# Performance work log

Measured on AMD Instinct MI355X. Metric: run time of the kernel, lower is better.

The kernel has to match this reference:

```python
import jax, jax.numpy as jnp
import numpy as np
import math

D, H = 128, 8
B, LC, LQ = 8, 512, 64


def pos_signal(channels, length):
    # tensor2tensor timing signal, returned as [C, L]
    pos = jnp.arange(length, dtype=jnp.float32)
    nts = channels // 2
    inc = math.log(1.0e4) / (nts - 1)
    inv = jnp.exp(jnp.arange(nts, dtype=jnp.float32) * -inc)
    st = pos[:, None] * inv[None, :]                      # [L, nts]
    sig = jnp.concatenate([jnp.sin(st), jnp.cos(st)], 1)  # [L, C]
    return sig.T


def mask_logits(t, m):
    return t * m + (1.0 - m) * -1e30


def ln_c(x, g, b):  # LayerNorm over channel dim of [B, D, L]
    mu = jnp.mean(x, axis=1, keepdims=True)
    var = jnp.mean((x - mu) ** 2, axis=1, keepdims=True)
    return (x - mu) / jnp.sqrt(var + 1e-5) * g[None, :, None] + b[None, :, None]


def conv1x1(x, w, b=None):  # x [B, I, L], w [O, I]
    y = jnp.einsum('oi,bil->bol', w, x)
    return y if b is None else y + b[None, :, None]


def dw_sep_conv(x, dw, pw, pwb):  # depthwise (k, no bias) -> pointwise (bias) -> relu
    k = dw.shape[-1]
    y = jax.lax.conv_general_dilated(x, dw[:, None, :], (1,), [(k // 2, k // 2)],
        dimension_numbers=('NCH', 'OIH', 'NCH'), feature_group_count=x.shape[1])
    return jax.nn.relu(conv1x1(y, pw, pwb))


def self_attention(x, mem_w, q_w, mask, n_head):  # x [B, D, L]
    b, d, L = x.shape
    dh = d // n_head
    mem = jnp.einsum('oi,bil->blo', mem_w, x)  # [B, L, 2D]
    q = jnp.einsum('oi,bil->blo', q_w, x)      # [B, L, D]
    def heads(t):
        return t.reshape(b, L, n_head, dh).transpose(0, 2, 1, 3)  # [B, H, L, dh]
    Qh = heads(q) * dh ** -0.5
    K = heads(mem[..., :d])
    V = heads(mem[..., d:])
    logits = jnp.einsum('bhqe,bhke->bhqk', Qh, K)
    logits = mask_logits(logits, mask[:, None, None, :])
    w = jax.nn.softmax(logits, axis=-1)
    o = jnp.einsum('bhqk,bhke->bhqe', w, V)
    return o.transpose(0, 2, 1, 3).reshape(b, L, d).transpose(0, 2, 1)


def encoder_block(x, mask, p, n_head):
    out = x + pos_signal(x.shape[1], x.shape[2])[None]
    n_conv = p['dw'].shape[0]
    for i in range(n_conv):
        res = out
        out = ln_c(out, p['lnc_g'][i], p['lnc_b'][i])
        out = dw_sep_conv(out, p['dw'][i], p['pw'][i], p['pw_b'][i]) + res
    res = out
    out = ln_c(out, p['ln1_g'], p['ln1_b'])
    out = self_attention(out, p['mem_w'], p['q_w'], mask, n_head) + res
    res = out
    out = ln_c(out, p['ln2_g'], p['ln2_b'])
    out = jax.nn.relu(conv1x1(out, p['ffn1_w'], p['ffn1_b']))
    out = conv1x1(out, p['ffn2_w'], p['ffn2_b'])
    return out + res


def cq_attention(Ce, Qe, cmask, qmask, w4C, w4Q, w4mlu, cq_b):
    Cx = Ce.transpose(0, 2, 1)   # [B, Lc, 2D]
    Qx = Qe.transpose(0, 2, 1)   # [B, Lq, 2D]
    s0 = jnp.einsum('bld,d->bl', Cx, w4C)[:, :, None]
    s1 = jnp.einsum('bqd,d->bq', Qx, w4Q)[:, None, :]
    s2 = jnp.einsum('bld,bqd->blq', Cx * w4mlu[None, None, :], Qx)
    S = s0 + s1 + s2 + cq_b
    S1 = jax.nn.softmax(mask_logits(S, qmask[:, None, :]), axis=2)
    S2 = jax.nn.softmax(mask_logits(S, cmask[:, :, None]), axis=1)
    A = jnp.einsum('blq,bqd->bld', S1, Qx)
    Bt = jnp.einsum('blq,bmq,bmd->bld', S1, S2, Cx)  # (S1 @ S2^T) @ C
    out = jnp.concatenate([Cx, A, Cx * A, Cx * Bt], axis=2)
    return out.transpose(0, 2, 1)  # [B, 8D, Lc]


def _forward(C, Q, maskC, maskQ, e_dw, e_pw, e_pw_b, e_lnc_g, e_lnc_b, e_mem_w, e_q_w,
             e_ffn1_w, e_ffn1_b, e_ffn2_w, e_ffn2_b, e_ln1_g, e_ln1_b, e_ln2_g, e_ln2_b,
             w4C, w4Q, w4mlu, cq_b, resizer_w,
             m_dw, m_pw, m_pw_b, m_lnc_g, m_lnc_b, m_mem_w, m_q_w,
             m_ffn1_w, m_ffn1_b, m_ffn2_w, m_ffn2_b, m_ln1_g, m_ln1_b, m_ln2_g, m_ln2_b):
    ep = dict(dw=e_dw, pw=e_pw, pw_b=e_pw_b, lnc_g=e_lnc_g, lnc_b=e_lnc_b,
              mem_w=e_mem_w, q_w=e_q_w, ffn1_w=e_ffn1_w, ffn1_b=e_ffn1_b,
              ffn2_w=e_ffn2_w, ffn2_b=e_ffn2_b, ln1_g=e_ln1_g, ln1_b=e_ln1_b,
              ln2_g=e_ln2_g, ln2_b=e_ln2_b)
    mp = dict(dw=m_dw, pw=m_pw, pw_b=m_pw_b, lnc_g=m_lnc_g, lnc_b=m_lnc_b,
              mem_w=m_mem_w, q_w=m_q_w, ffn1_w=m_ffn1_w, ffn1_b=m_ffn1_b,
              ffn2_w=m_ffn2_w, ffn2_b=m_ffn2_b, ln1_g=m_ln1_g, ln1_b=m_ln1_b,
              ln2_g=m_ln2_g, ln2_b=m_ln2_b)
    Ce = encoder_block(C, maskC, ep, H)
    Qe = encoder_block(Q, maskQ, ep, H)
    Ce = jnp.concatenate([Ce, C], axis=1)  # encode_fusion -> [B, 2D, Lc]
    Qe = jnp.concatenate([Qe, Q], axis=1)
    X = cq_attention(Ce, Qe, maskC, maskQ, w4C, w4Q, w4mlu, cq_b)
    X = jnp.concatenate([X, Ce], axis=1)   # match_fusion -> [B, 10D, Lc]
    M0 = conv1x1(X, resizer_w)             # [B, D, Lc]

    def run(m):
        def step(carry, p):
            return encoder_block(carry, maskC, p, H), None
        m, _ = jax.lax.scan(step, m, mp)
        return m

    M1 = run(M0)
    M2 = run(M1)
    M3 = run(M2)
    return M1, M2, M3


def setup_inputs() -> dict:
    key = jax.random.key(0)
    ks = iter(jax.random.split(key, 48))
    def rn(shape, scale):
        return jax.random.normal(next(ks), shape, dtype=jnp.float32) * scale
    s1 = 1.0 / math.sqrt(D)
    s2 = 1.0 / math.sqrt(2 * D)
    f32 = jnp.float32
    return dict(
        C=rn((B, D, LC), 1.0), Q=rn((B, D, LQ), 1.0),
        maskC=jnp.ones((B, LC), f32), maskQ=jnp.ones((B, LQ), f32),
        e_dw=rn((4, D, 7), 1.0 / math.sqrt(7)), e_pw=rn((4, D, D), s1),
        e_pw_b=jnp.zeros((4, D), f32), e_lnc_g=jnp.ones((4, D), f32), e_lnc_b=jnp.zeros((4, D), f32),
        e_mem_w=rn((2 * D, D), s1), e_q_w=rn((D, D), s1),
        e_ffn1_w=rn((D, D), s1), e_ffn1_b=jnp.zeros((D,), f32),
        e_ffn2_w=rn((D, D), s1), e_ffn2_b=jnp.zeros((D,), f32),
        e_ln1_g=jnp.ones((D,), f32), e_ln1_b=jnp.zeros((D,), f32),
        e_ln2_g=jnp.ones((D,), f32), e_ln2_b=jnp.zeros((D,), f32),
        w4C=rn((2 * D,), s2), w4Q=rn((2 * D,), s2), w4mlu=rn((2 * D,), s2),
        cq_b=jnp.zeros((1,), f32),
        resizer_w=rn((D, 10 * D), 1.0 / math.sqrt(10 * D)),
        m_dw=rn((7, 2, D, 5), 1.0 / math.sqrt(5)), m_pw=rn((7, 2, D, D), s1),
        m_pw_b=jnp.zeros((7, 2, D), f32), m_lnc_g=jnp.ones((7, 2, D), f32), m_lnc_b=jnp.zeros((7, 2, D), f32),
        m_mem_w=rn((7, 2 * D, D), s1), m_q_w=rn((7, D, D), s1),
        m_ffn1_w=rn((7, D, D), s1), m_ffn1_b=jnp.zeros((7, D), f32),
        m_ffn2_w=rn((7, D, D), s1), m_ffn2_b=jnp.zeros((7, D), f32),
        m_ln1_g=jnp.ones((7, D), f32), m_ln1_b=jnp.zeros((7, D), f32),
        m_ln2_g=jnp.ones((7, D), f32), m_ln2_b=jnp.zeros((7, D), f32),
    )


def reference(C, Q, maskC, maskQ, e_dw, e_pw, e_pw_b, e_lnc_g, e_lnc_b, e_mem_w, e_q_w,
              e_ffn1_w, e_ffn1_b, e_ffn2_w, e_ffn2_b, e_ln1_g, e_ln1_b, e_ln2_g, e_ln2_b,
              w4C, w4Q, w4mlu, cq_b, resizer_w,
              m_dw, m_pw, m_pw_b, m_lnc_g, m_lnc_b, m_mem_w, m_q_w,
              m_ffn1_w, m_ffn1_b, m_ffn2_w, m_ffn2_b, m_ln1_g, m_ln1_b, m_ln2_g, m_ln2_b):
    return _forward(C, Q, maskC, maskQ, e_dw, e_pw, e_pw_b, e_lnc_g, e_lnc_b, e_mem_w, e_q_w,
                    e_ffn1_w, e_ffn1_b, e_ffn2_w, e_ffn2_b, e_ln1_g, e_ln1_b, e_ln2_g, e_ln2_b,
                    w4C, w4Q, w4mlu, cq_b, resizer_w,
                    m_dw, m_pw, m_pw_b, m_lnc_g, m_lnc_b, m_mem_w, m_q_w,
                    m_ffn1_w, m_ffn1_b, m_ffn2_w, m_ffn2_b, m_ln1_g, m_ln1_b, m_ln2_g, m_ln2_b)
```

## Files before the change

### kernel.cpp

```cpp
#include <hip/hip_runtime.h>
#include <math.h>

#define D_  128
#define B_  8
#define H_  8
#define LC_ 512
#define LQ_ 64

typedef float f32x4 __attribute__((ext_vector_type(4)));
typedef short bf16x8 __attribute__((ext_vector_type(8)));
typedef short short4v __attribute__((ext_vector_type(4)));
typedef unsigned short ushortT;

__device__ inline short bfr(float x) {
  unsigned u = __float_as_uint(x);
  u += 0x7fff + ((u >> 16) & 1);
  return (short)(u >> 16);
}
__device__ inline float bfi(ushortT u) {
  return __uint_as_float(((unsigned)u) << 16);
}

__device__ inline bf16x8 mk8(short4v lo, short4v hi) {
  bf16x8 r;
  r[0] = lo[0]; r[1] = lo[1]; r[2] = lo[2]; r[3] = lo[3];
  r[4] = hi[0]; r[5] = hi[1]; r[6] = hi[2]; r[7] = hi[3];
  return r;
}

__device__ inline bf16x8 ldA(const ushortT* row, int koff) {
  short4v lo = *(const short4v*)(row + koff);
  short4v hi = *(const short4v*)(row + koff + 16);
  return mk8(lo, hi);
}
__device__ inline bf16x8 ldB2(const ushortT* plo, const ushortT* phi) {
  short4v lo = *(const short4v*)plo;
  short4v hi = *(const short4v*)phi;
  return mk8(lo, hi);
}

__global__ void k_prep(const float* a0, const float* a1, const float* a2,
                       const float* a3, const float* a4, const float* a5,
                       const float* a6, const float* a7, const float* a8,
                       const float* a9, const float* a10, ushortT* dst) {
  int i = blockIdx.x * 256 + threadIdx.x;
  if (i >= 1114112) return;
  const float* s; int lo;
  if      (i <   65536) { s = a0;  lo = i; }
  else if (i <   98304) { s = a1;  lo = i - 65536; }
  else if (i <  114688) { s = a2;  lo = i - 98304; }
  else if (i <  131072) { s = a3;  lo = i - 114688; }
  else if (i <  147456) { s = a4;  lo = i - 131072; }
  else if (i <  311296) { s = a5;  lo = i - 147456; }
  else if (i <  540672) { s = a6;  lo = i - 311296; }
  else if (i <  770048) { s = a7;  lo = i - 540672; }
  else if (i <  884736) { s = a8;  lo = i - 770048; }
  else if (i <  999424) { s = a9;  lo = i - 884736; }
  else                  { s = a10; lo = i - 999424; }
  dst[i] = (ushortT)bfr(s[lo]);
}

template <int KK, int ADDPOS>
__global__ __launch_bounds__(256) void k_fusedconv(
    const float* __restrict__ xC, float* __restrict__ yC,
    const float* __restrict__ xQ, float* __restrict__ yQ,
    const float* __restrict__ dw1, const ushortT* __restrict__ pw1,
    const float* __restrict__ pb1, const float* __restrict__ g1,
    const float* __restrict__ be1,
    const float* __restrict__ dw2, const ushortT* __restrict__ pw2,
    const float* __restrict__ pb2, const float* __restrict__ g2w,
    const float* __restrict__ be2, int ntC) {
  const int HALO = KK / 2;
  const int W1 = 32 + 2 * HALO;
  __shared__ __align__(16) float raw[128 * 40];
  __shared__ __align__(16) ushortT l1o[128 * 36];
  __shared__ __align__(16) ushortT xbf1[32 * 32 * 4];
  __shared__ float mu1[40], rs1[40], mu2[32], rs2[32], ps[160], psq[160];
  ushortT* xbf2 = (ushortT*)raw;
  int bx = blockIdx.x;
  const float* x; float* yout; int l0, L;
  if (bx < ntC) { x = xC; yout = yC; l0 = bx * 16; L = LC_; }
  else          { x = xQ; yout = yQ; l0 = (bx - ntC) * 16; L = LQ_; }
  int o0 = blockIdx.y * 64;
  int b = blockIdx.z;
  int tid = threadIdx.x;
  for (int idx = tid; idx < 128 * W1; idx += 256) {
    int d = idx / W1, c = idx - d * W1;
    int gl = l0 - 8 - HALO + c;
    float v = 0.f;
    if (gl >= 0 && gl < L) {
      v = x[((size_t)b * 128 + d) * L + gl];
      if (ADDPOS) {
        int j = d & 63;
        float arg = (float)gl * expf(-(float)j * 0.14619588f);
        v += (d < 64) ? sinf(arg) : cosf(arg);
      }
    }
    raw[d * 40 + c] = v;
  }
  __syncthreads();
  if (tid < 4 * W1) {
    int c = tid % W1, hh = tid / W1;
    float s = 0.f, s2 = 0.f;
    for (int d = hh * 32; d < hh * 32 + 32; d++) {
      float v = raw[d * 40 + c];
      s += v; s2 += v * v;
    }
    ps[tid] = s; psq[tid] = s2;
  }
  __syncthreads();
  if (tid < W1) {
    float s = ps[tid] + ps[tid + W1] + ps[tid + 2 * W1] + ps[tid + 3 * W1];
    float s2 = psq[tid] + psq[tid + W1] + psq[tid + 2 * W1] + psq[tid + 3 * W1];
    float mu = s * (1.f / 128.f);
    float var = fmaxf(s2 * (1.f / 128.f) - mu * mu, 0.f);
    mu1[tid] = mu; rs1[tid] = rsqrtf(var + 1e-5f);
  }
  __syncthreads();
  {
    int cc0 = tid & 31, dbase = tid >> 5;
#pragma unroll
    for (int kq = 0; kq < 4; kq++) {
      short4v pk;
#pragma unroll
      for (int e = 0; e < 4; e++) {
        int d = dbase * 16 + kq * 4 + e;
        float gg = g1[d], bb = be1[d];
        const float* wr = dw1 + d * KK;
        float acc = 0.f;
#pragma unroll
        for (int t = 0; t < KK; t++) {
          int ci = cc0 + t;
          int gl = l0 - 8 - HALO + ci;
          float lv = 0.f;
          if (gl >= 0 && gl < L)
            lv = (raw[d * 40 + ci] - mu1[ci]) * rs1[ci] * gg + bb;
          acc += wr[t] * lv;
        }
        pk[e] = bfr(acc);
      }
      *(short4v*)&xbf1[(((dbase * 4 + kq) * 32) + cc0) * 4] = pk;
    }
  }
  __syncthreads();
  int w = tid >> 6, lane = tid & 63, g2 = lane >> 4, r = lane & 15;
  {
    f32x4 acc[2][2];
#pragma unroll
    for (int i = 0; i < 2; i++)
#pragma unroll
      for (int nt = 0; nt < 2; nt++) acc[i][nt] = (f32x4){0.f, 0.f, 0.f, 0.f};
#pragma unroll
    for (int i = 0; i < 2; i++) {
      const ushortT* arow = pw1 + (size_t)((2 * w + i) * 16 + r) * 128;
#pragma unroll
      for (int kk = 0; kk < 4; kk++) {
        bf16x8 a = ldA(arow, kk * 32 + g2 * 4);
#pragma unroll
        for (int nt = 0; nt < 2; nt++) {
          bf16x8 bb = ldB2(&xbf1[(((kk * 8 + g2) * 32) + nt * 16 + r) * 4],
                           &xbf1[(((kk * 8 + 4 + g2) * 32) + nt * 16 + r) * 4]);
          acc[i][nt] = __builtin_amdgcn_mfma_f32_16x16x32_bf16(a, bb, acc[i][nt], 0, 0, 0);
        }
      }
    }
#pragma unroll
    for (int i = 0; i < 2; i++)
#pragma unroll
      for (int nt = 0; nt < 2; nt++)
#pragma unroll
        for (int p = 0; p < 4; p++) {
          int o = (2 * w + i) * 16 + g2 * 4 + p;
          int c1 = nt * 16 + r;
          int gl = l0 - 8 + c1;
          float val = 0.f;
          if (gl >= 0 && gl < L)
            val = fmaxf(acc[i][nt][p] + pb1[o], 0.f) + raw[o * 40 + c1 + HALO];
          l1o[o * 36 + c1] = (ushortT)bfr(val);
        }
  }
  __syncthreads();
  if (tid < 128) {
    int c = tid & 31, hh = tid >> 5;
    float s = 0.f, s2 = 0.f;
    for (int d = hh * 32; d < hh * 32 + 32; d++) {
      float v = bfi(l1o[d * 36 + c]);
      s += v; s2 += v * v;
    }
    ps[tid] = s; psq[tid] = s2;
  }
  __syncthreads();
  if (tid < 32) {
    float s = ps[tid] + ps[tid + 32] + ps[tid + 64] + ps[tid + 96];
    float s2 = psq[tid] + psq[tid + 32] + psq[tid + 64] + psq[tid + 96];
    float mu = s * (1.f / 128.f);
    float var = fmaxf(s2 * (1.f / 128.f) - mu * mu, 0.f);
    mu2[tid] = mu; rs2[tid] = rsqrtf(var + 1e-5f);
  }
  __syncthreads();
  {
    int cc2 = tid & 15, db2 = tid >> 4;
#pragma unroll
    for (int kq = 0; kq < 2; kq++) {
      short4v pk;
#pragma unroll
      for (int e = 0; e < 4; e++) {
        int d = db2 * 8 + kq * 4 + e;
        float gg = g2w[d], bb = be2[d];
        const float* wr = dw2 + d * KK;
        float acc = 0.f;
#pragma unroll
        for (int t = 0; t < KK; t++) {
          int c1 = cc2 + 8 + t - HALO;
          int gl = l0 + cc2 + t - HALO;
          float lv = 0.f;
          if (gl >= 0 && gl < L)
            lv = (bfi(l1o[d * 36 + c1]) - mu2[c1]) * rs2[c1] * gg + bb;
          acc += wr[t] * lv;
        }
        pk[e] = bfr(acc);
      }
      *(short4v*)&xbf2[(((db2 * 2 + kq) * 16) + cc2) * 4] = pk;
    }
  }
  __syncthreads();
  {
    f32x4 a2 = {0.f, 0.f, 0.f, 0.f};
    const ushortT* arow = pw2 + (size_t)(o0 + 16 * w + r) * 128;
#pragma unroll
    for (int kk = 0; kk < 4; kk++) {
      bf16x8 a = ldA(arow, kk * 32 + g2 * 4);
      bf16x8 bb = ldB2(&xbf2[(((kk * 8 + g2) * 16) + r) * 4],
                       &xbf2[(((kk * 8 + 4 + g2) * 16) + r) * 4]);
      a2 = __builtin_amdgcn_mfma_f32_16x16x32_bf16(a, bb, a2, 0, 0, 0);
    }
#pragma unroll
    for (int p = 0; p < 4; p++) {
      int o = o0 + 16 * w + g2 * 4 + p;
      yout[((size_t)b * 128 + o) * L + l0 + r] =
          fmaxf(a2[p] + pb2[o], 0.f) + bfi(l1o[o * 36 + 8 + r]);
    }
  }
}

template <int KK, int ADDPOS>
__global__ __launch_bounds__(1024) void k_convproj1024(
    const float* __restrict__ xC, float* __restrict__ yC,
    float* __restrict__ mkvC, float* __restrict__ qpC,
    const float* __restrict__ xQ, float* __restrict__ yQ,
    float* __restrict__ mkvQ, float* __restrict__ qpQ,
    const float* __restrict__ dw1, const ushortT* __restrict__ pw1,
    const float* __restrict__ pb1, const float* __restrict__ g1,
    const float* __restrict__ be1,
    const float* __restrict__ dw2, const ushortT* __restrict__ pw2,
    const float* __restrict__ pb2, const float* __restrict__ g2w,
    const float* __restrict__ be2,
    const ushortT* __restrict__ memw, const ushortT* __restrict__ qw,
    const float* __restrict__ g3, const float* __restrict__ be3, int ntC) {
  const int HALO = KK / 2;
  const int W1 = 32 + 2 * HALO;
  __shared__ __align__(16) float raw[128 * 40];
  __shared__ __align__(16) ushortT l1o[128 * 36];
  __shared__ __align__(16) ushortT xbf1[32 * 32 * 4];
  __shared__ __align__(16) ushortT c2o[128 * 16];
  __shared__ float mu1[40], rs1[40], mu2[32], rs2[32], mu3[16], rs3[16];
  __shared__ float ps[160], psq[160];
  ushortT* xbf2 = (ushortT*)raw;
  ushortT* xbf3 = (ushortT*)(raw + 4096);
  int bx = blockIdx.x;
  const float* x; float* yout; float* mkv; float* qp; int l0, L;
  if (bx < ntC) { x = xC; yout = yC; mkv = mkvC; qp = qpC; l0 = bx * 16; L = LC_; }
  else          { x = xQ; yout = yQ; mkv = mkvQ; qp = qpQ; l0 = (bx - ntC) * 16; L = LQ_; }
  int b = blockIdx.z;
  int tid = threadIdx.x;
  for (int idx = tid; idx < 128 * W1; idx += 1024) {
    int d = idx / W1, c = idx - d * W1;
    int gl = l0 - 8 - HALO + c;
    float v = 0.f;
    if (gl >= 0 && gl < L) {
      v = x[((size_t)b * 128 + d) * L + gl];
      if (ADDPOS) {
        int j = d & 63;
        float arg = (float)gl * expf(-(float)j * 0.14619588f);
        v += (d < 64) ? sinf(arg) : cosf(arg);
      }
    }
    raw[d * 40 + c] = v;
  }
  __syncthreads();
  if (tid < 4 * W1) {
    int c = tid % W1, hh = tid / W1;
    float s = 0.f, s2 = 0.f;
    for (int d = hh * 32; d < hh * 32 + 32; d++) {
      float v = raw[d * 40 + c];
      s += v; s2 += v * v;
    }
    ps[tid] = s; psq[tid] = s2;
  }
  __syncthreads();
  if (tid < W1) {
    float s = ps[tid] + ps[tid + W1] + ps[tid + 2 * W1] + ps[tid + 3 * W1];
    float s2 = psq[tid] + psq[tid + W1] + psq[tid + 2 * W1] + psq[tid + 3 * W1];
    float mu = s * (1.f / 128.f);
    float var = fmaxf(s2 * (1.f / 128.f) - mu * mu, 0.f);
    mu1[tid] = mu; rs1[tid] = rsqrtf(var + 1e-5f);
  }
  __syncthreads();
  {
    int cc0 = tid & 31, dbase = tid >> 5;
    short4v pk;
#pragma unroll
    for (int e = 0; e < 4; e++) {
      int d = dbase * 4 + e;
      float gg = g1[d], bb = be1[d];
      const float* wr = dw1 + d * KK;
      float acc = 0.f;
#pragma unroll
      for (int t = 0; t < KK; t++) {
        int ci = cc0 + t;
        int gl = l0 - 8 - HALO + ci;
        float lv = 0.f;
        if (gl >= 0 && gl < L)
          lv = (raw[d * 40 + ci] - mu1[ci]) * rs1[ci] * gg + bb;
        acc += wr[t] * lv;
      }
      pk[e] = bfr(acc);
    }
    *(short4v*)&xbf1[((dbase * 32) + cc0) * 4] = pk;
  }
  __syncthreads();
  int w = tid >> 6, lane = tid & 63, g2 = lane >> 4, r = lane & 15;
  {
    int m = w & 7, nt = w >> 3;
    f32x4 acc = {0.f, 0.f, 0.f, 0.f};
    const ushortT* arow = pw1 + (size_t)(m * 16 + r) * 128;
#pragma unroll
    for (int kk = 0; kk < 4; kk++) {
      bf16x8 a = ldA(arow, kk * 32 + g2 * 4);
      bf16x8 bb = ldB2(&xbf1[(((kk * 8 + g2) * 32) + nt * 16 + r) * 4],
                       &xbf1[(((kk * 8 + 4 + g2) * 32) + nt * 16 + r) * 4]);
      acc = __builtin_amdgcn_mfma_f32_16x16x32_bf16(a, bb, acc, 0, 0, 0);
    }
#pragma unroll
    for (int p = 0; p < 4; p++) {
      int o = m * 16 + g2 * 4 + p;
      int c1 = nt * 16 + r;
      int gl = l0 - 8 + c1;
      float val = 0.f;
      if (gl >= 0 && gl < L)
        val = fmaxf(acc[p] + pb1[o], 0.f) + raw[o * 40 + c1 + HALO];
      l1o[o * 36 + c1] = (ushortT)bfr(val);
    }
  }
  __syncthreads();
  if (tid < 128) {
    int c = tid & 31, hh = tid >> 5;
    float s = 0.f, s2 = 0.f;
    for (int d = hh * 32; d < hh * 32 + 32; d++) {
      float v = bfi(l1o[d * 36 + c]);
      s += v; s2 += v * v;
    }
    ps[tid] = s; psq[tid] = s2;
  }
  __syncthreads();
  if (tid < 32) {
    float s = ps[tid] + ps[tid + 32] + ps[tid + 64] + ps[tid + 96];
    float s2 = psq[tid] + psq[tid + 32] + psq[tid + 64] + psq[tid + 96];
    float mu = s * (1.f / 128.f);
    float var = fmaxf(s2 * (1.f / 128.f) - mu * mu, 0.f);
    mu2[tid] = mu; rs2[tid] = rsqrtf(var + 1e-5f);
  }
  __syncthreads();
  {
    int cc2 = tid & 15, db2 = tid >> 4;
#pragma unroll
    for (int e = 0; e < 2; e++) {
      int d = db2 * 2 + e;
      float gg = g2w[d], bb = be2[d];
      const float* wr = dw2 + d * KK;
      float acc = 0.f;
#pragma unroll
      for (int t = 0; t < KK; t++) {
        int c1 = cc2 + 8 + t - HALO;
        int gl = l0 + cc2 + t - HALO;
        float lv = 0.f;
        if (gl >= 0 && gl < L)
          lv = (bfi(l1o[d * 36 + c1]) - mu2[c1]) * rs2[c1] * gg + bb;
        acc += wr[t] * lv;
      }
      xbf2[(((d >> 2) * 16) + cc2) * 4 + (d & 3)] = (ushortT)bfr(acc);
    }
  }
  __syncthreads();
  if (w < 8) {
    f32x4 a2 = {0.f, 0.f, 0.f, 0.f};
    const ushortT* arow = pw2 + (size_t)(w * 16 + r) * 128;
#pragma unroll
    for (int kk = 0; kk < 4; kk++) {
      bf16x8 a = ldA(arow, kk * 32 + g2 * 4);
      bf16x8 bb = ldB2(&xbf2[(((kk * 8 + g2) * 16) + r) * 4],
                       &xbf2[(((kk * 8 + 4 + g2) * 16) + r) * 4]);
      a2 = __builtin_amdgcn_mfma_f32_16x16x32_bf16(a, bb, a2, 0, 0, 0);
    }
#pragma unroll
    for (int p = 0; p < 4; p++) {
      int o = w * 16 + g2 * 4 + p;
      float val = fmaxf(a2[p] + pb2[o], 0.f) + bfi(l1o[o * 36 + 8 + r]);
      yout[((size_t)b * 128 + o) * L + l0 + r] = val;
      c2o[o * 16 + r] = (ushortT)bfr(val);
    }
  }
  __syncthreads();
  if (tid < 128) {
    int c = tid & 15, hh = tid >> 4;
    float s = 0.f, s2 = 0.f;
    for (int d = hh * 16; d < hh * 16 + 16; d++) {
      float v = bfi(c2o[d * 16 + c]);
      s += v; s2 += v * v;
    }
    ps[tid] = s; psq[tid] = s2;
  }
  __syncthreads();
  if (tid < 16) {
    float s = 0.f, s2 = 0.f;
#pragma unroll
    for (int hh = 0; hh < 8; hh++) { s += ps[hh * 16 + tid]; s2 += psq[hh * 16 + tid]; }
    float mu = s * (1.f / 128.f);
    float var = fmaxf(s2 * (1.f / 128.f) - mu * mu, 0.f);
    mu3[tid] = mu; rs3[tid] = rsqrtf(var + 1e-5f);
  }
  __syncthreads();
  for (int idx = tid; idx < 2048; idx += 1024) {
    int d = idx >> 4, c = idx & 15;
    float val = (bfi(c2o[d * 16 + c]) - mu3[c]) * rs3[c] * g3[d] + be3[d];
    xbf3[(((d >> 2) * 16) + c) * 4 + (d & 3)] = (ushortT)bfr(val);
  }
  __syncthreads();
#pragma unroll
  for (int t = 0; t < 2; t++) {
    int mt = w + 16 * t;
    if (mt < 24) {
      const ushortT* arow; float* outp; int obase, O;
      if (mt < 16) { arow = memw + (size_t)(mt * 16 + r) * 128; outp = mkv; obase = mt * 16; O = 256; }
      else         { arow = qw + (size_t)((mt - 16) * 16 + r) * 128; outp = qp; obase = (mt - 16) * 16; O = 128; }
      f32x4 acc = {0.f, 0.f, 0.f, 0.f};
#pragma unroll
      for (int kk = 0; kk < 4; kk++) {
        bf16x8 a = ldA(arow, kk * 32 + g2 * 4);
        bf16x8 bb = ldB2(&xbf3[(((kk * 8 + g2) * 16) + r) * 4],
                         &xbf3[(((kk * 8 + 4 + g2) * 16) + r) * 4]);
        acc = __builtin_amdgcn_mfma_f32_16x16x32_bf16(a, bb, acc, 0, 0, 0);
      }
#pragma unroll
      for (int p = 0; p < 4; p++)
        outp[((size_t)b * O + obase + g2 * 4 + p) * L + l0 + r] = acc[p];
    }
  }
}

template <int NCH, int WOUT>
__device__ __forceinline__ void attn_body(
    char* smem, const float* memKV, const float* qp, const float* mask,
    float* cur, const ushortT* w1bf, const float* b1,
    const ushortT* w2bf, const float* b2,
    const float* g, const float* be, float* wout, int q0, int b, int L, int tid) {
  float* msh = (float*)smem;
  float* ssh = (float*)(smem + 2048);
  float* OshF = (float*)(smem + 4096);
  float* updT = (float*)(smem + 12288);
  ushortT* xbf = (ushortT*)(smem + 20480);
  ushortT* midbf = (ushortT*)(smem + 24576);
  float* mu_s = (float*)(smem + 28672);
  float* rs_s = (float*)(smem + 28736);
  float* ps = (float*)(smem + 28800);
  float* psq = (float*)(smem + 32896);
  int w = tid >> 6;
  int h = w & 7, kh = w >> 3;
  int lane = tid & 63;
  int g2 = lane >> 4, r = lane & 15;
  const float* qb = qp + ((size_t)b * 128 + h * 16) * L;
  const float* kb = memKV + ((size_t)b * 256 + h * 16) * L;
  const float* vb = memKV + ((size_t)b * 256 + 128 + h * 16) * L;
  const float* mk = mask + (size_t)b * L;
  int qcol = q0 + r;
  bf16x8 qf;
#pragma unroll
  for (int j = 0; j < 4; j++)
    qf[j] = bfr(qb[(size_t)(g2 * 4 + j) * L + qcol] * 0.25f);
  qf[4] = 0; qf[5] = 0; qf[6] = 0; qf[7] = 0;
  float m_run = -INFINITY, ssum = 0.f;
  f32x4 O = {0.f, 0.f, 0.f, 0.f};
  int kbeg = kh * (L / 2), kend = (kh + 1) * (L / 2);
  for (int k0 = kbeg; k0 < kend; k0 += NCH * 16) {
    f32x4 sd[NCH];
#pragma unroll
    for (int mc = 0; mc < NCH; mc++) {
      bf16x8 kf;
      int krow = k0 + mc * 16 + r;
#pragma unroll
      for (int j = 0; j < 4; j++)
        kf[j] = bfr(kb[(size_t)(g2 * 4 + j) * L + krow]);
      kf[4] = 0; kf[5] = 0; kf[6] = 0; kf[7] = 0;
      f32x4 z = {0.f, 0.f, 0.f, 0.f};
      sd[mc] = __builtin_amdgcn_mfma_f32_16x16x32_bf16(kf, qf, z, 0, 0, 0);
    }
    float tm = -INFINITY;
#pragma unroll
    for (int mc = 0; mc < NCH; mc++) {
#pragma unroll
      for (int p = 0; p < 4; p++) {
        float mv = mk[k0 + mc * 16 + g2 * 4 + p];
        float sv = sd[mc][p] * mv + (1.f - mv) * (-1e30f);
        sd[mc][p] = sv;
        tm = fmaxf(tm, sv);
      }
    }
    tm = fmaxf(tm, __shfl_xor(tm, 16));
    tm = fmaxf(tm, __shfl_xor(tm, 32));
    float nm = fmaxf(m_run, tm);
    float c = __expf(m_run - nm);
    ssum *= c;
    O[0] *= c; O[1] *= c; O[2] *= c; O[3] *= c;
    float psum = 0.f;
    bf16x8 pf[NCH / 2];
#pragma unroll
    for (int c2 = 0; c2 < NCH / 2; c2++) {
#pragma unroll
      for (int j = 0; j < 4; j++) {
        float e0 = __expf(sd[2 * c2][j] - nm);
        float e1 = __expf(sd[2 * c2 + 1][j] - nm);
        psum += e0 + e1;
        pf[c2][j] = bfr(e0);
        pf[c2][j + 4] = bfr(e1);
      }
    }
    psum += __shfl_xor(psum, 16);
    psum += __shfl_xor(psum, 32);
    ssum += psum;
#pragma unroll
    for (int c2 = 0; c2 < NCH / 2; c2++) {
      const float* vrow = vb + (size_t)r * L + k0 + c2 * 32 + g2 * 4;
      float4 v0 = *(const float4*)vrow;
      float4 v1 = *(const float4*)(vrow + 16);
      bf16x8 vf;
      vf[0] = bfr(v0.x); vf[1] = bfr(v0.y); vf[2] = bfr(v0.z); vf[3] = bfr(v0.w);
      vf[4] = bfr(v1.x); vf[5] = bfr(v1.y); vf[6] = bfr(v1.z); vf[7] = bfr(v1.w);
      O = __builtin_amdgcn_mfma_f32_16x16x32_bf16(vf, pf[c2], O, 0, 0, 0);
    }
    m_run = nm;
  }
  if (kh == 1) {
    msh[h * 64 + lane] = m_run;
    ssh[h * 64 + lane] = ssum;
#pragma unroll
    for (int p = 0; p < 4; p++) OshF[(h * 64 + lane) * 4 + p] = O[p];
  }
  __syncthreads();
  if (kh == 0) {
    float mB = msh[h * 64 + lane], sB = ssh[h * 64 + lane];
    float nm = fmaxf(m_run, mB);
    float cA = __expf(m_run - nm), cB = __expf(mB - nm);
    float inv = 1.f / (ssum * cA + sB * cB);
#pragma unroll
    for (int p = 0; p < 4; p++) {
      int d = h * 16 + g2 * 4 + p;
      float ov = (O[p] * cA + OshF[(h * 64 + lane) * 4 + p] * cB) * inv;
      updT[d * 16 + r] = cur[((size_t)b * 128 + d) * L + qcol] + ov;
    }
  }
  __syncthreads();
  {
    int c = tid & 15, hh = tid >> 4;
    float s = 0.f, s2 = 0.f;
    for (int d = hh * 2; d < hh * 2 + 2; d++) {
      float v = updT[d * 16 + c];
      s += v; s2 += v * v;
    }
    ps[tid] = s; psq[tid] = s2;
  }
  __syncthreads();
  if (tid < 16) {
    float s = 0.f, s2 = 0.f;
    for (int hh = 0; hh < 64; hh++) { s += ps[hh * 16 + tid]; s2 += psq[hh * 16 + tid]; }
    float mu = s * (1.f / 128.f);
    float var = fmaxf(s2 * (1.f / 128.f) - mu * mu, 0.f);
    mu_s[tid] = mu; rs_s[tid] = rsqrtf(var + 1e-5f);
  }
  __syncthreads();
  for (int idx = tid; idx < 2048; idx += 1024) {
    int d = idx >> 4, c = idx & 15;
    float val = (updT[d * 16 + c] - mu_s[c]) * rs_s[c] * g[d] + be[d];
    xbf[(((d >> 2) * 16) + c) * 4 + (d & 3)] = (ushortT)bfr(val);
  }
  __syncthreads();
  if (w < 8) {
    f32x4 acc = {0.f, 0.f, 0.f, 0.f};
    const ushortT* ar = w1bf + (size_t)(16 * w + r) * 128;
#pragma unroll
    for (int kk = 0; kk < 4; kk++) {
      bf16x8 a = ldA(ar, kk * 32 + g2 * 4);
      bf16x8 bb = ldB2(&xbf[(((kk * 8 + g2) * 16) + r) * 4],
                       &xbf[(((kk * 8 + 4 + g2) * 16) + r) * 4]);
      acc = __builtin_amdgcn_mfma_f32_16x16x32_bf16(a, bb, acc, 0, 0, 0);
    }
#pragma unroll
    for (int p = 0; p < 4; p++) {
      int dmid = 16 * w + g2 * 4 + p;
      float val = fmaxf(acc[p] + b1[dmid], 0.f);
      midbf[(((4 * w + g2) * 16) + r) * 4 + p] = (ushortT)bfr(val);
    }
  }
  __syncthreads();
  if (w < 8) {
    f32x4 a2 = {0.f, 0.f, 0.f, 0.f};
    const ushortT* ar = w2bf + (size_t)(16 * w + r) * 128;
#pragma unroll
    for (int kk = 0; kk < 4; kk++) {
      bf16x8 a = ldA(ar, kk * 32 + g2 * 4);
      bf16x8 bb = ldB2(&midbf[(((kk * 8 + g2) * 16) + r) * 4],
                       &midbf[(((kk * 8 + 4 + g2) * 16) + r) * 4]);
      a2 = __builtin_amdgcn_mfma_f32_16x16x32_bf16(a, bb, a2, 0, 0, 0);
    }
#pragma unroll
    for (int p = 0; p < 4; p++) {
      int o = 16 * w + g2 * 4 + p;
      size_t pos = ((size_t)b * 128 + o) * L + q0 + r;
      float val = a2[p] + b2[o] + updT[o * 16 + r];
      cur[pos] = val;
      if (WOUT) wout[pos] = val;
    }
  }
}

template <int WOUT>
__global__ __launch_bounds__(1024) void k_attnffn_m(
    const float* memKV, const float* qp, const float* mask, float* cur,
    const ushortT* w1bf, const float* b1, const ushortT* w2bf, const float* b2,
    const float* g, const float* be, float* wout) {
  __shared__ __align__(16) char smem[36992];
  attn_body<8, WOUT>(smem, memKV, qp, mask, cur, w1bf, b1, w2bf, b2, g, be,
                     wout, blockIdx.x * 16, blockIdx.z, LC_, threadIdx.x);
}

__global__ __launch_bounds__(1024) void k_attnffn_in(
    const float* mkvC, const float* qpC, const float* maskC, float* curC,
    const float* mkvQ, const float* qpQ, const float* maskQ, float* curQ,
    const ushortT* w1bf, const float* b1, const ushortT* w2bf, const float* b2,
    const float* g, const float* be, int ntC) {
  __shared__ __align__(16) char smem[36992];
  int bx = blockIdx.x;
  if (bx < ntC)
    attn_body<8, 0>(smem, mkvC, qpC, maskC, curC, w1bf, b1, w2bf, b2, g, be,
                    nullptr, bx * 16, blockIdx.z, LC_, threadIdx.x);
  else
    attn_body<2, 0>(smem, mkvQ, qpQ, maskQ, curQ, w1bf, b1, w2bf, b2, g, be,
                    nullptr, (bx - ntC) * 16, blockIdx.z, LQ_, threadIdx.x);
}


__global__ void k_concat2m(const float* __restrict__ x1C, const float* __restrict__ x2C,
                           float* __restrict__ outC,
                           const float* __restrict__ x1Q, const float* __restrict__ x2Q,
                           float* __restrict__ outQ) {
  int idx = blockIdx.x * 256 + threadIdx.x;
  const int tot1 = B_ * 256 * LC_;
  const int tot2 = B_ * 256 * LQ_;
  if (idx < tot1) {
    int l = idx % LC_;
    int c = (idx / LC_) & 255;
    int b = idx / (LC_ * 256);
    float v = (c < 128) ? x1C[((size_t)b * 128 + c) * LC_ + l]
                        : x2C[((size_t)b * 128 + (c - 128)) * LC_ + l];
    outC[idx] = v;
  } else {
    int i2 = idx - tot1;
    if (i2 < tot2) {
      int l = i2 % LQ_;
      int c = (i2 / LQ_) & 255;
      int b = i2 / (LQ_ * 256);
      float v = (c < 128) ? x1Q[((size_t)b * 128 + c) * LQ_ + l]
                          : x2Q[((size_t)b * 128 + (c - 128)) * LQ_ + l];
      outQ[i2] = v;
    }
  }
}

__global__ void k_cqSrow(const float* __restrict__ Ce, const float* __restrict__ Qe,
                         const float* __restrict__ w4C, const float* __restrict__ w4Q,
                         const float* __restrict__ w4mlu, const float* __restrict__ cqb,
                         const float* __restrict__ qmask,
                         float* __restrict__ S, float* __restrict__ S1) {
  int idx = blockIdx.x * 256 + threadIdx.x;
  int q = idx & 63;
  int l = (idx >> 6) % LC_;
  int b = (idx >> 6) / LC_;
  const float* ce = Ce + (size_t)b * 256 * LC_ + l;
  const float* qe = Qe + (size_t)b * 256 * LQ_ + q;
  float acc = 0.f, a0 = 0.f, a1 = 0.f;
#pragma unroll 8
  for (int j = 0; j < 256; j++) {
    float cv = ce[(size_t)j * LC_];
    float qv = qe[(size_t)j * LQ_];
    acc += cv * w4mlu[j] * qv;
    a0 += cv * w4C[j];
    a1 += qv * w4Q[j];
  }
  float sv = acc + a0 + a1 + cqb[0];
  S[idx] = sv;
  float mv = qmask[b * LQ_ + q];
  float v = sv * mv + (1.f - mv) * (-1e30f);
  float mx = v;
  for (int off = 32; off; off >>= 1) mx = fmaxf(mx, __shfl_xor(mx, off));
  float p = expf(v - mx);
  float s = p;
  for (int off = 32; off; off >>= 1) s += __shfl_xor(s, off);
  S1[idx] = p / s;
}

__global__ __launch_bounds__(256) void k_softmax_col(
    const float* __restrict__ S, const float* __restrict__ cmask, float* __restrict__ S2) {
  int q = blockIdx.x & 63, b = blockIdx.x >> 6;
  int tid = threadIdx.x;
  __shared__ float redm[4], reds[4];
  const float* col = S + (size_t)b * LC_ * LQ_ + q;
  const float* mk = cmask + b * LC_;
  float vm[2];
#pragma unroll
  for (int k = 0; k < 2; k++) {
    int l = tid + 256 * k;
// ... 69 lines not shown
  int w = tid >> 6, lane = tid & 63, g2 = lane >> 4, r = lane & 15;
  const ushortT* arow = wbf + (size_t)(16 * w + r) * 1280;
  f32x4 acc = {0.f, 0.f, 0.f, 0.f};
  for (int kt = 0; kt < 1280; kt += 128) {
    __syncthreads();
    for (int idx = tid; idx < 2048; idx += 512) {
      int kl = idx >> 4, cc = idx & 15;
      int ch = kt + kl;
      int seg = ch >> 8;
      int j = ch & 255;
      size_t p = ((size_t)b * 256 + j) * LC_ + l0 + cc;
      float v;
      if (seg == 0 || seg == 4) v = Ce[p];
      else if (seg == 1) v = A[p];
      else if (seg == 2) v = Ce[p] * A[p];
      else v = Ce[p] * Bt[p];
      xbf[((kl >> 2) * 16 + cc) * 4 + (kl & 3)] = (ushortT)bfr(v);
    }
    __syncthreads();
#pragma unroll
    for (int kk2 = 0; kk2 < 4; kk2++) {
      bf16x8 a = ldA(arow, kt + kk2 * 32 + g2 * 4);
      bf16x8 b0 = ldB2(&xbf[(((kk2 * 8 + g2) * 16) + r) * 4],
                       &xbf[(((kk2 * 8 + 4 + g2) * 16) + r) * 4]);
      acc = __builtin_amdgcn_mfma_f32_16x16x32_bf16(a, b0, acc, 0, 0, 0);
    }
  }
#pragma unroll
  for (int p = 0; p < 4; p++) {
    int o = 16 * w + g2 * 4 + p;
    y[((size_t)b * D_ + o) * LC_ + l0 + r] = acc[p];
  }
}


extern "C" void kernel_launch(void* const* d_in, const int* in_sizes, int n_in,
                              void* d_out, int out_size, void* d_ws, size_t ws_size,
                              hipStream_t stream) {
  (void)in_sizes; (void)n_in; (void)out_size; (void)ws_size;
  const float* C        = (const float*)d_in[0];
  const float* Q        = (const float*)d_in[1];
  const float* maskC    = (const float*)d_in[2];
  const float* maskQ    = (const float*)d_in[3];
  const float* e_dw     = (const float*)d_in[4];
  const float* e_pw     = (const float*)d_in[5];
  const float* e_pw_b   = (const float*)d_in[6];
  const float* e_lnc_g  = (const float*)d_in[7];
  const float* e_lnc_b  = (const float*)d_in[8];
  const float* e_mem_w  = (const float*)d_in[9];
  const float* e_q_w    = (const float*)d_in[10];
  const float* e_ffn1_w = (const float*)d_in[11];
  const float* e_ffn1_b = (const float*)d_in[12];
  const float* e_ffn2_w = (const float*)d_in[13];
  const float* e_ffn2_b = (const float*)d_in[14];
  const float* e_ln1_g  = (const float*)d_in[15];
  const float* e_ln1_b  = (const float*)d_in[16];
  const float* e_ln2_g  = (const float*)d_in[17];
  const float* e_ln2_b  = (const float*)d_in[18];
  const float* w4C      = (const float*)d_in[19];
  const float* w4Q      = (const float*)d_in[20];
  const float* w4mlu    = (const float*)d_in[21];
  const float* cq_b     = (const float*)d_in[22];
  const float* resizer_w= (const float*)d_in[23];
  const float* m_dw     = (const float*)d_in[24];
  const float* m_pw     = (const float*)d_in[25];
  const float* m_pw_b   = (const float*)d_in[26];
  const float* m_lnc_g  = (const float*)d_in[27];
  const float* m_lnc_b  = (const float*)d_in[28];
  const float* m_mem_w  = (const float*)d_in[29];
  const float* m_q_w    = (const float*)d_in[30];
  const float* m_ffn1_w = (const float*)d_in[31];
  const float* m_ffn1_b = (const float*)d_in[32];
  const float* m_ffn2_w = (const float*)d_in[33];
  const float* m_ffn2_b = (const float*)d_in[34];
  const float* m_ln1_g  = (const float*)d_in[35];
  const float* m_ln1_b  = (const float*)d_in[36];
  const float* m_ln2_g  = (const float*)d_in[37];
  const float* m_ln2_b  = (const float*)d_in[38];

  float* ws = (float*)d_ws;
  const size_t SB = (size_t)B_ * D_ * LC_;
  float* cur  = ws;
  float* aux  = cur + SB;
  float* mkv  = aux + SB;
  float* qpb  = mkv + 2 * SB;
  float* Ce   = qpb + SB;
  float* Qe   = Ce + 2 * SB;
  float* Sbuf = Qe + (size_t)B_ * 256 * LQ_;
  float* S1   = Sbuf + (size_t)B_ * LC_ * LQ_;
  float* S2   = S1 + (size_t)B_ * LC_ * LQ_;
  float* Yb   = S2 + (size_t)B_ * LC_ * LQ_;
  float* Mb   = Yb + (size_t)B_ * 256 * LQ_;
  float* Ab   = mkv;
  float* Bb   = cur;
  ushortT* wb = (ushortT*)(Mb + SB);
  ushortT* w_epw  = wb;
  ushortT* w_emem = wb + 65536;
  ushortT* w_eq   = wb + 98304;
  ushortT* w_ef1  = wb + 114688;
  ushortT* w_ef2  = wb + 131072;
  ushortT* w_rsz  = wb + 147456;
  ushortT* w_mpw  = wb + 311296;
  ushortT* w_mmem = wb + 540672;
  ushortT* w_mq   = wb + 770048;
  ushortT* w_mf1  = wb + 884736;
  ushortT* w_mf2  = wb + 999424;
  float* after_wb = (float*)(wb + 1114112);
  float* curQ  = after_wb;
  float* auxQ  = curQ + 65536;
  float* mkvQ  = auxQ + 65536;
  float* qpbQ  = mkvQ + 131072;

  k_prep<<<(1114112 + 255) / 256, 256, 0, stream>>>(
      e_pw, e_mem_w, e_q_w, e_ffn1_w, e_ffn2_w, resizer_w,
      m_pw, m_mem_w, m_q_w, m_ffn1_w, m_ffn2_w, wb);

  k_fusedconv<7, 1><<<dim3(36, 2, B_), 256, 0, stream>>>(
      C, cur, Q, curQ,
      e_dw + 0 * 896, w_epw + 0, e_pw_b + 0, e_lnc_g + 0, e_lnc_b + 0,
      e_dw + 1 * 896, w_epw + 16384, e_pw_b + 128, e_lnc_g + 128, e_lnc_b + 128, 32);
  k_convproj1024<7, 0><<<dim3(36, 1, B_), 1024, 0, stream>>>(
      cur, aux, mkv, qpb, curQ, auxQ, mkvQ, qpbQ,
      e_dw + 2 * 896, w_epw + 32768, e_pw_b + 256, e_lnc_g + 256, e_lnc_b + 256,
      e_dw + 3 * 896, w_epw + 49152, e_pw_b + 384, e_lnc_g + 384, e_lnc_b + 384,
      w_emem, w_eq, e_ln1_g, e_ln1_b, 32);
  k_attnffn_in<<<dim3(36, 1, B_), 1024, 0, stream>>>(
      mkv, qpb, maskC, aux, mkvQ, qpbQ, maskQ, auxQ,
      w_ef1, e_ffn1_b, w_ef2, e_ffn2_b, e_ln2_g, e_ln2_b, 32);
  k_concat2m<<<(B_ * 256 * (LC_ + LQ_) + 255) / 256, 256, 0, stream>>>(
      aux, C, Ce, auxQ, Q, Qe);

  k_cqSrow<<<(B_ * LC_ * LQ_) / 256, 256, 0, stream>>>(Ce, Qe, w4C, w4Q, w4mlu, cq_b, maskQ, Sbuf, S1);
  k_softmax_col<<<B_ * LQ_, 256, 0, stream>>>(Sbuf, maskC, S2);
  k_cqY<<<(B_ * 256 * LQ_) / 256, 256, 0, stream>>>(S2, Ce, Yb);
  k_cqAB<<<dim3(LC_ / 64, 64, B_), 256, 0, stream>>>(S1, Qe, Yb, Ab, Bb);
  k_resizer512<<<dim3(LC_ / 16, 1, B_), 512, 0, stream>>>(Ce, Ab, Bb, w_rsz, Mb);

  float* out = (float*)d_out;
  float* bufs[2] = {cur, aux};
  int cb = 0;
  const float* src = Mb;
  for (int r = 0; r < 3; r++) {
    for (int bi = 0; bi < 7; bi++) {
      int pc0 = bi * 2, pc1 = bi * 2 + 1;
      float* ob = bufs[cb];
      k_convproj1024<5, 1><<<dim3(32, 1, B_), 1024, 0, stream>>>(
          src, ob, mkv, qpb, src, ob, mkv, qpb,
          m_dw + (size_t)pc0 * 640, w_mpw + (size_t)pc0 * 16384, m_pw_b + pc0 * 128,
          m_lnc_g + pc0 * 128, m_lnc_b + pc0 * 128,
          m_dw + (size_t)pc1 * 640, w_mpw + (size_t)pc1 * 16384, m_pw_b + pc1 * 128,
          m_lnc_g + pc1 * 128, m_lnc_b + pc1 * 128,
          w_mmem + (size_t)bi * 32768, w_mq + (size_t)bi * 16384,
          m_ln1_g + bi * 128, m_ln1_b + bi * 128, 32);
      if (bi == 6)
        k_attnffn_m<1><<<dim3(32, 1, B_), 1024, 0, stream>>>(
            mkv, qpb, maskC, ob,
            w_mf1 + (size_t)bi * 16384, m_ffn1_b + bi * 128,
            w_mf2 + (size_t)bi * 16384, m_ffn2_b + bi * 128,
            m_ln2_g + bi * 128, m_ln2_b + bi * 128, out + (size_t)r * SB);
      else
        k_attnffn_m<0><<<dim3(32, 1, B_), 1024, 0, stream>>>(
            mkv, qpb, maskC, ob,
            w_mf1 + (size_t)bi * 16384, m_ffn1_b + bi * 128,
            w_mf2 + (size_t)bi * 16384, m_ffn2_b + bi * 128,
            m_ln2_g + bi * 128, m_ln2_b + bi * 128, nullptr);
      src = ob;
      cb ^= 1;
    }
  }
}
```

Before: 1.335 ms.

## Store K/V/Q projections as bf16 and precompute positional signal table

The projection kernels now write the memory (K/V) and query projections as bf16 instead of fp32, and the attention kernel reads them directly as bf16 MFMA operands without per-element conversion. This halves the intermediate traffic between the projection and attention kernels across all 21 model-encoder blocks plus the embedding encoder. The sinusoidal position signal is also computed once into a table by a new kernel, so the conv kernels load it instead of calling expf, sinf and cosf per element. The FFN warp index is recomputed from tid with renamed locals. Rounding now happens once at the store, which matches the rounding the attention path already applied.

```diff
diff --git a/kernel.cpp b/kernel.cpp
--- a/kernel.cpp
+++ b/kernel.cpp
@@ -60,10 +60,19 @@
   dst[i] = (ushortT)bfr(s[lo]);
 }
 
+__global__ void k_postab(float* pos) {
+  int i = blockIdx.x * 256 + threadIdx.x;
+  int d = i >> 9, l = i & 511;
+  int j = d & 63;
+  float arg = (float)l * expf(-(float)j * 0.14619588f);
+  pos[i] = (d < 64) ? sinf(arg) : cosf(arg);
+}
+
 template <int KK, int ADDPOS>
 __global__ __launch_bounds__(256) void k_fusedconv(
     const float* __restrict__ xC, float* __restrict__ yC,
     const float* __restrict__ xQ, float* __restrict__ yQ,
+    const float* __restrict__ pos,
     const float* __restrict__ dw1, const ushortT* __restrict__ pw1,
     const float* __restrict__ pb1, const float* __restrict__ g1,
     const float* __restrict__ be1,
@@ -90,11 +99,7 @@
     float v = 0.f;
     if (gl >= 0 && gl < L) {
       v = x[((size_t)b * 128 + d) * L + gl];
-      if (ADDPOS) {
-        int j = d & 63;
-        float arg = (float)gl * expf(-(float)j * 0.14619588f);
-        v += (d < 64) ? sinf(arg) : cosf(arg);
-      }
+      if (ADDPOS) v += pos[d * 512 + gl];
     }
     raw[d * 40 + c] = v;
   }
@@ -246,9 +251,10 @@
 template <int KK, int ADDPOS>
 __global__ __launch_bounds__(1024) void k_convproj1024(
     const float* __restrict__ xC, float* __restrict__ yC,
-    float* __restrict__ mkvC, float* __restrict__ qpC,
+    ushortT* __restrict__ mkvC, ushortT* __restrict__ qpC,
     const float* __restrict__ xQ, float* __restrict__ yQ,
-    float* __restrict__ mkvQ, float* __restrict__ qpQ,
+    ushortT* __restrict__ mkvQ, ushortT* __restrict__ qpQ,
+    const float* __restrict__ pos,
     const float* __restrict__ dw1, const ushortT* __restrict__ pw1,
     const float* __restrict__ pb1, const float* __restrict__ g1,
     const float* __restrict__ be1,
@@ -268,7 +274,7 @@
   ushortT* xbf2 = (ushortT*)raw;
   ushortT* xbf3 = (ushortT*)(raw + 4096);
   int bx = blockIdx.x;
-  const float* x; float* yout; float* mkv; float* qp; int l0, L;
+  const float* x; float* yout; ushortT* mkv; ushortT* qp; int l0, L;
   if (bx < ntC) { x = xC; yout = yC; mkv = mkvC; qp = qpC; l0 = bx * 16; L = LC_; }
   else          { x = xQ; yout = yQ; mkv = mkvQ; qp = qpQ; l0 = (bx - ntC) * 16; L = LQ_; }
   int b = blockIdx.z;
@@ -279,11 +285,7 @@
     float v = 0.f;
     if (gl >= 0 && gl < L) {
       v = x[((size_t)b * 128 + d) * L + gl];
-      if (ADDPOS) {
-        int j = d & 63;
-        float arg = (float)gl * expf(-(float)j * 0.14619588f);
-        v += (d < 64) ? sinf(arg) : cosf(arg);
-      }
+      if (ADDPOS) v += pos[d * 512 + gl];
     }
     raw[d * 40 + c] = v;
   }
@@ -440,7 +442,7 @@
   for (int t = 0; t < 2; t++) {
     int mt = w + 16 * t;
     if (mt < 24) {
-      const ushortT* arow; float* outp; int obase, O;
+      const ushortT* arow; ushortT* outp; int obase, O;
       if (mt < 16) { arow = memw + (size_t)(mt * 16 + r) * 128; outp = mkv; obase = mt * 16; O = 256; }
       else         { arow = qw + (size_t)((mt - 16) * 16 + r) * 128; outp = qp; obase = (mt - 16) * 16; O = 128; }
       f32x4 acc = {0.f, 0.f, 0.f, 0.f};
@@ -453,14 +455,14 @@
       }
 #pragma unroll
       for (int p = 0; p < 4; p++)
-        outp[((size_t)b * O + obase + g2 * 4 + p) * L + l0 + r] = acc[p];
+        outp[((size_t)b * O + obase + g2 * 4 + p) * L + l0 + r] = (ushortT)bfr(acc[p]);
     }
   }
 }
 
 template <int NCH, int WOUT>
 __device__ __forceinline__ void attn_body(
-    char* smem, const float* memKV, const float* qp, const float* mask,
+    char* smem, const ushortT* memKV, const ushortT* qp, const float* mask,
     float* cur, const ushortT* w1bf, const float* b1,
     const ushortT* w2bf, const float* b2,
     const float* g, const float* be, float* wout, int q0, int b, int L, int tid) {
@@ -478,15 +480,15 @@
   int h = w & 7, kh = w >> 3;
   int lane = tid & 63;
   int g2 = lane >> 4, r = lane & 15;
-  const float* qb = qp + ((size_t)b * 128 + h * 16) * L;
-  const float* kb = memKV + ((size_t)b * 256 + h * 16) * L;
-  const float* vb = memKV + ((size_t)b * 256 + 128 + h * 16) * L;
+  const ushortT* qb = qp + ((size_t)b * 128 + h * 16) * L;
+  const ushortT* kb = memKV + ((size_t)b * 256 + h * 16) * L;
+  const ushortT* vb = memKV + ((size_t)b * 256 + 128 + h * 16) * L;
   const float* mk = mask + (size_t)b * L;
   int qcol = q0 + r;
   bf16x8 qf;
 #pragma unroll
   for (int j = 0; j < 4; j++)
-    qf[j] = bfr(qb[(size_t)(g2 * 4 + j) * L + qcol] * 0.25f);
+    qf[j] = bfr(bfi(qb[(size_t)(g2 * 4 + j) * L + qcol]) * 0.25f);
   qf[4] = 0; qf[5] = 0; qf[6] = 0; qf[7] = 0;
   float m_run = -INFINITY, ssum = 0.f;
   f32x4 O = {0.f, 0.f, 0.f, 0.f};
@@ -499,7 +501,7 @@
       int krow = k0 + mc * 16 + r;
 #pragma unroll
       for (int j = 0; j < 4; j++)
-        kf[j] = bfr(kb[(size_t)(g2 * 4 + j) * L + krow]);
+        kf[j] = (short)kb[(size_t)(g2 * 4 + j) * L + krow];
       kf[4] = 0; kf[5] = 0; kf[6] = 0; kf[7] = 0;
       f32x4 z = {0.f, 0.f, 0.f, 0.f};
       sd[mc] = __builtin_amdgcn_mfma_f32_16x16x32_bf16(kf, qf, z, 0, 0, 0);
@@ -539,12 +541,10 @@
     ssum += psum;
 #pragma unroll
     for (int c2 = 0; c2 < NCH / 2; c2++) {
-      const float* vrow = vb + (size_t)r * L + k0 + c2 * 32 + g2 * 4;
-      float4 v0 = *(const float4*)vrow;
-      float4 v1 = *(const float4*)(vrow + 16);
-      bf16x8 vf;
-      vf[0] = bfr(v0.x); vf[1] = bfr(v0.y); vf[2] = bfr(v0.z); vf[3] = bfr(v0.w);
-      vf[4] = bfr(v1.x); vf[5] = bfr(v1.y); vf[6] = bfr(v1.z); vf[7] = bfr(v1.w);
+      const ushortT* vrow = vb + (size_t)r * L + k0 + c2 * 32 + g2 * 4;
+      short4v lo = *(const short4v*)vrow;
+      short4v hi = *(const short4v*)(vrow + 16);
+      bf16x8 vf = mk8(lo, hi);
       O = __builtin_amdgcn_mfma_f32_16x16x32_bf16(vf, pf[c2], O, 0, 0, 0);
     }
     m_run = nm;
@@ -593,48 +593,50 @@
     xbf[(((d >> 2) * 16) + c) * 4 + (d & 3)] = (ushortT)bfr(val);
   }
   __syncthreads();
-  if (w < 8) {
+  int w8 = tid >> 6;
+  int g2b = (tid & 63) >> 4, rb = tid & 15;
+  if (w8 < 8) {
     f32x4 acc = {0.f, 0.f, 0.f, 0.f};
-    const ushortT* ar = w1bf + (size_t)(16 * w + r) * 128;
+    const ushortT* ar = w1bf + (size_t)(16 * w8 + rb) * 128;
 #pragma unroll
     for (int kk = 0; kk < 4; kk++) {
-      bf16x8 a = ldA(ar, kk * 32 + g2 * 4);
-      bf16x8 bb = ldB2(&xbf[(((kk * 8 + g2) * 16) + r) * 4],
-                       &xbf[(((kk * 8 + 4 + g2) * 16) + r) * 4]);
+      bf16x8 a = ldA(ar, kk * 32 + g2b * 4);
+      bf16x8 bb = ldB2(&xbf[(((kk * 8 + g2b) * 16) + rb) * 4],
+                       &xbf[(((kk * 8 + 4 + g2b) * 16) + rb) * 4]);
       acc = __builtin_amdgcn_mfma_f32_16x16x32_bf16(a, bb, acc, 0, 0, 0);
     }
 #pragma unroll
     for (int p = 0; p < 4; p++) {
-      int dmid = 16 * w + g2 * 4 + p;
+      int dmid = 16 * w8 + g2b * 4 + p;
       float val = fmaxf(acc[p] + b1[dmid], 0.f);
-      midbf[(((4 * w + g2) * 16) + r) * 4 + p] = (ushortT)bfr(val);
-    }
-  }
-  __syncthreads();
-  if (w < 8) {
+      midbf[(((4 * w8 + g2b) * 16) + rb) * 4 + p] = (ushortT)bfr(val);
+    }
+  }
+  __syncthreads();
+  if (w8 < 8) {
     f32x4 a2 = {0.f, 0.f, 0.f, 0.f};
-    const ushortT* ar = w2bf + (size_t)(16 * w + r) * 128;
+    const ushortT* ar = w2bf + (size_t)(16 * w8 + rb) * 128;
 #pragma unroll
     for (int kk = 0; kk < 4; kk++) {
-      bf16x8 a = ldA(ar, kk * 32 + g2 * 4);
-      bf16x8 bb = ldB2(&midbf[(((kk * 8 + g2) * 16) + r) * 4],
-                       &midbf[(((kk * 8 + 4 + g2) * 16) + r) * 4]);
+      bf16x8 a = ldA(ar, kk * 32 + g2b * 4);
+      bf16x8 bb = ldB2(&midbf[(((kk * 8 + g2b) * 16) + rb) * 4],
+                       &midbf[(((kk * 8 + 4 + g2b) * 16) + rb) * 4]);
       a2 = __builtin_amdgcn_mfma_f32_16x16x32_bf16(a, bb, a2, 0, 0, 0);
     }
 #pragma unroll
     for (int p = 0; p < 4; p++) {
-      int o = 16 * w + g2 * 4 + p;
-      size_t pos = ((size_t)b * 128 + o) * L + q0 + r;
-      float val = a2[p] + b2[o] + updT[o * 16 + r];
-      cur[pos] = val;
-      if (WOUT) wout[pos] = val;
+      int o = 16 * w8 + g2b * 4 + p;
+      size_t pos2 = ((size_t)b * 128 + o) * L + q0 + rb;
+      float val = a2[p] + b2[o] + updT[o * 16 + rb];
+      cur[pos2] = val;
+      if (WOUT) wout[pos2] = val;
     }
   }
 }
 
 template <int WOUT>
 __global__ __launch_bounds__(1024) void k_attnffn_m(
-    const float* memKV, const float* qp, const float* mask, float* cur,
+    const ushortT* memKV, const ushortT* qp, const float* mask, float* cur,
     const ushortT* w1bf, const float* b1, const ushortT* w2bf, const float* b2,
     const float* g, const float* be, float* wout) {
   __shared__ __align__(16) char smem[36992];
@@ -643,8 +645,8 @@
 }
 
 __global__ __launch_bounds__(1024) void k_attnffn_in(
-    const float* mkvC, const float* qpC, const float* maskC, float* curC,
-    const float* mkvQ, const float* qpQ, const float* maskQ, float* curQ,
+    const ushortT* mkvC, const ushortT* qpC, const float* maskC, float* curC,
+    const ushortT* mkvQ, const ushortT* qpQ, const float* maskQ, float* curQ,
     const ushortT* w1bf, const float* b1, const ushortT* w2bf, const float* b2,
     const float* g, const float* be, int ntC) {
   __shared__ __align__(16) char smem[36992];
@@ -880,17 +882,19 @@
   const size_t SB = (size_t)B_ * D_ * LC_;
   float* cur  = ws;
   float* aux  = cur + SB;
-  float* mkv  = aux + SB;
-  float* qpb  = mkv + 2 * SB;
-  float* Ce   = qpb + SB;
+  float* mkvF = aux + SB;
+  float* qpbF = mkvF + 2 * SB;
+  float* Ce   = qpbF + SB;
   float* Qe   = Ce + 2 * SB;
   float* Sbuf = Qe + (size_t)B_ * 256 * LQ_;
   float* S1   = Sbuf + (size_t)B_ * LC_ * LQ_;
   float* S2   = S1 + (size_t)B_ * LC_ * LQ_;
   float* Yb   = S2 + (size_t)B_ * LC_ * LQ_;
   float* Mb   = Yb + (size_t)B_ * 256 * LQ_;
-  float* Ab   = mkv;
+  float* Ab   = mkvF;
   float* Bb   = cur;
+  ushortT* mkvB = (ushortT*)mkvF;
+  ushortT* qpbB = (ushortT*)qpbF;
   ushortT* wb = (ushortT*)(Mb + SB);
   ushortT* w_epw  = wb;
   ushortT* w_emem = wb + 65536;
@@ -906,24 +910,26 @@
   float* after_wb = (float*)(wb + 1114112);
   float* curQ  = after_wb;
   float* auxQ  = curQ + 65536;
-  float* mkvQ  = auxQ + 65536;
-  float* qpbQ  = mkvQ + 131072;
+  ushortT* mkvQB = (ushortT*)(auxQ + 65536);
+  ushortT* qpbQB = (ushortT*)(auxQ + 131072);
+  float* posT  = auxQ + 196608;
 
   k_prep<<<(1114112 + 255) / 256, 256, 0, stream>>>(
       e_pw, e_mem_w, e_q_w, e_ffn1_w, e_ffn2_w, resizer_w,
       m_pw, m_mem_w, m_q_w, m_ffn1_w, m_ffn2_w, wb);
+  k_postab<<<256, 256, 0, stream>>>(posT);
 
   k_fusedconv<7, 1><<<dim3(36, 2, B_), 256, 0, stream>>>(
-      C, cur, Q, curQ,
+      C, cur, Q, curQ, posT,
       e_dw + 0 * 896, w_epw + 0, e_pw_b + 0, e_lnc_g + 0, e_lnc_b + 0,
       e_dw + 1 * 896, w_epw + 16384, e_pw_b + 128, e_lnc_g + 128, e_lnc_b + 128, 32);
   k_convproj1024<7, 0><<<dim3(36, 1, B_), 1024, 0, stream>>>(
-      cur, aux, mkv, qpb, curQ, auxQ, mkvQ, qpbQ,
+      cur, aux, mkvB, qpbB, curQ, auxQ, mkvQB, qpbQB, posT,
       e_dw + 2 * 896, w_epw + 32768, e_pw_b + 256, e_lnc_g + 256, e_lnc_b + 256,
       e_dw + 3 * 896, w_epw + 49152, e_pw_b + 384, e_lnc_g + 384, e_lnc_b + 384,
       w_emem, w_eq, e_ln1_g, e_ln1_b, 32);
   k_attnffn_in<<<dim3(36, 1, B_), 1024, 0, stream>>>(
-      mkv, qpb, maskC, aux, mkvQ, qpbQ, maskQ, auxQ,
+      mkvB, qpbB, maskC, aux, mkvQB, qpbQB, maskQ, auxQ,
       w_ef1, e_ffn1_b, w_ef2, e_ffn2_b, e_ln2_g, e_ln2_b, 32);
   k_concat2m<<<(B_ * 256 * (LC_ + LQ_) + 255) / 256, 256, 0, stream>>>(
       aux, C, Ce, auxQ, Q, Qe);
@@ -943,7 +949,7 @@
       int pc0 = bi * 2, pc1 = bi * 2 + 1;
       float* ob = bufs[cb];
       k_convproj1024<5, 1><<<dim3(32, 1, B_), 1024, 0, stream>>>(
-          src, ob, mkv, qpb, src, ob, mkv, qpb,
+          src, ob, mkvB, qpbB, src, ob, mkvB, qpbB, posT,
           m_dw + (size_t)pc0 * 640, w_mpw + (size_t)pc0 * 16384, m_pw_b + pc0 * 128,
           m_lnc_g + pc0 * 128, m_lnc_b + pc0 * 128,
           m_dw + (size_t)pc1 * 640, w_mpw + (size_t)pc1 * 16384, m_pw_b + pc1 * 128,
@@ -952,13 +958,13 @@
           m_ln1_g + bi * 128, m_ln1_b + bi * 128, 32);
       if (bi == 6)
         k_attnffn_m<1><<<dim3(32, 1, B_), 1024, 0, stream>>>(
-            mkv, qpb, maskC, ob,
+            mkvB, qpbB, maskC, ob,
             w_mf1 + (size_t)bi * 16384, m_ffn1_b + bi * 128,
             w_mf2 + (size_t)bi * 16384, m_ffn2_b + bi * 128,
             m_ln2_g + bi * 128, m_ln2_b + bi * 128, out + (size_t)r * SB);
       else
         k_attnffn_m<0><<<dim3(32, 1, B_), 1024, 0, stream>>>(
-            mkv, qpb, maskC, ob,
+            mkvB, qpbB, maskC, ob,
             w_mf1 + (size_t)bi * 16384, m_ffn1_b + bi * 128,
             w_mf2 + (size_t)bi * 16384, m_ffn2_b + bi * 128,
             m_ln2_g + bi * 128, m_ln2_b + bi * 128, nullptr);
```

After: 1.241 ms, median of 3. 7.0% less time.
